# Kernel optimization log

Hardware: AMD Instinct MI355X
Metric: run time of the kernel (lower is better)

The kernel has to match this reference:

```python
import jax, jax.numpy as jnp
import numpy as np

RADIUS = 0.2
NSAMPLE = 32
USE_XYZ = True
NORMALIZE_XYZ = False


def setup_inputs() -> dict:
    key = jax.random.key(0)
    k1, k2, k3 = jax.random.split(key, 3)
    B, N, S, C = 4, 8192, 2048, 64
    xyz = jax.random.uniform(k1, (B, N, 3), dtype=jnp.float32)
    new_xyz = jax.random.uniform(k2, (B, S, 3), dtype=jnp.float32)
    features = jax.random.normal(k3, (B, C, N), dtype=jnp.float32)
    return {"xyz": xyz, "new_xyz": new_xyz, "features": features}


def _ball_query(new_xyz, xyz, radius, nsample):
    # squared distances [B, S, N] via ||q||^2 + ||p||^2 - 2 q.p (no [B,S,N,3] blowup)
    q2 = jnp.sum(new_xyz * new_xyz, axis=-1)  # [B, S]
    p2 = jnp.sum(xyz * xyz, axis=-1)          # [B, N]
    qp = jnp.einsum('bsd,bnd->bsn', new_xyz, xyz)
    d2 = q2[:, :, None] + p2[:, None, :] - 2.0 * qp
    N = xyz.shape[1]
    in_ball = d2 < radius * radius
    # CUDA ball_query semantics: first nsample indices (in original point order)
    # inside the ball; unfilled slots replicate the first found index.
    scores = jnp.where(in_ball, jnp.arange(N, dtype=jnp.int32), jnp.int32(N))
    sorted_idx = -jax.lax.top_k(-scores, nsample)[0]  # ascending smallest scores
    first = sorted_idx[..., :1]
    idx = jnp.where(sorted_idx < N, sorted_idx, first)
    idx = jnp.where(first < N, idx, 0)  # no neighbors at all -> index 0
    return idx  # [B, S, nsample] int32


def _group(features, idx):
    # features [B, C, N], idx [B, S, K] -> [B, C, S, K]
    return jax.vmap(lambda f, i: f[:, i])(features, idx)


def reference(xyz, new_xyz, features):
    idx = _ball_query(new_xyz, xyz, RADIUS, NSAMPLE)
    xyz_t = jnp.transpose(xyz, (0, 2, 1))  # [B, 3, N]
    grouped_xyz = _group(xyz_t, idx)  # [B, 3, S, K]
    grouped_xyz = grouped_xyz - jnp.transpose(new_xyz, (0, 2, 1))[..., None]
    if NORMALIZE_XYZ:
        grouped_xyz = grouped_xyz / RADIUS
    grouped_features = _group(features, idx)  # [B, C, S, K]
    if USE_XYZ:
        return jnp.concatenate([grouped_xyz, grouped_features], axis=1)
    return grouped_features
```

## Files before the change

kernel.cpp:

```cpp
#include <hip/hip_runtime.h>
#include <hip/hip_bf16.h>
#include <stdint.h>

#define BB 4
#define NN 8192
#define SS 2048
#define CC 64
#define NS 32

typedef unsigned short ushort8 __attribute__((ext_vector_type(8)));

__device__ __forceinline__ unsigned short f2bf(float f) {
    union { float ff; unsigned int i; } v; v.ff = f;
    unsigned int x = v.i;
    x += 0x7fffu + ((x >> 16) & 1u);
    return (unsigned short)(x >> 16);
}
__device__ __forceinline__ float bf2f(unsigned short u) {
    union { unsigned int i; float f; } v; v.i = ((unsigned int)u) << 16; return v.f;
}

__global__ void stage(const float* __restrict__ xyz,
                      const float* __restrict__ feat,
                      float4* __restrict__ pts,
                      unsigned short* __restrict__ ft) {
#pragma clang fp contract(off)
    const int t = threadIdx.x;
    if (blockIdx.x < 128) {
        int i = blockIdx.x * 256 + t;
        const float* p = xyz + (size_t)i * 3;
        float x = p[0], y = p[1], z = p[2];
        float p2 = x * x;
        p2 += y * y;
        p2 += z * z;
        pts[i] = make_float4(x, y, z, p2);
        return;
    }
    __shared__ float tile[64][65];
    const int blk = blockIdx.x - 128;
    const int b  = blk >> 7;
    const int n0 = (blk & 127) * 64;
    const float* fb = feat + (size_t)b * CC * NN;
    const int n = t & 63;
    #pragma unroll
    for (int it = 0; it < 16; ++it) {
        int c = it * 4 + (t >> 6);
        tile[n][c] = fb[(size_t)c * NN + n0 + n];
    }
    __syncthreads();
    unsigned short* fo = ft + ((size_t)b * NN + n0) * CC;
    const int c = t & 63;
    #pragma unroll
    for (int it = 0; it < 16; ++it) {
        int r = it * 4 + (t >> 6);
        fo[(size_t)r * CC + c] = f2bf(tile[r][c]);
    }
}

__launch_bounds__(256)
__global__ void bq_group(const float* __restrict__ new_xyz,
                         const float4* __restrict__ pts,
                         const unsigned short* __restrict__ ft,
                         float* __restrict__ out) {
#pragma clang fp contract(off)
    __shared__ unsigned long long wmask[2][4];
    __shared__ int sidx[NS];
    const int t    = threadIdx.x;
    const int wave = t >> 6;
    const int lane = t & 63;
    const int blk  = blockIdx.x;
    const int b    = blk >> 11;
    const int s    = blk & (SS - 1);

    const float* q = new_xyz + (size_t)(b * SS + s) * 3;
    const float qx = q[0], qy = q[1], qz = q[2];
    const float4* pb = pts + (size_t)b * NN;

    float q2 = qx * qx;
    q2 += qy * qy;
    q2 += qz * qz;

    const unsigned long long below = (1ull << lane) - 1ull;
    int have = 0;
    float4 p = pb[t];
    #pragma unroll 1
    for (int base = 0; base < NN; base += 256) {
        float4 pn = pb[(base + 256 < NN) ? (base + 256 + t) : t];
        float qp = qx * p.x;
        qp += qy * p.y;
        qp += qz * p.z;
        float t1 = q2 + p.w;
        float d2 = t1 - 2.0f * qp;
        bool in = d2 < 0.04f;
        unsigned long long m = __ballot(in);
        const int buf = (base >> 8) & 1;
        if (lane == 0) wmask[buf][wave] = m;
        __syncthreads();
        unsigned long long m0 = wmask[buf][0], m1 = wmask[buf][1],
                           m2 = wmask[buf][2], m3 = wmask[buf][3];
        int pre = __popcll(m & below);
        if (wave > 0) pre += __popcll(m0);
        if (wave > 1) pre += __popcll(m1);
        if (wave > 2) pre += __popcll(m2);
        int pos = have + pre;
        if (in && pos < NS) sidx[pos] = base + t;
        have += __popcll(m0) + __popcll(m1) + __popcll(m2) + __popcll(m3);
        if (have >= NS) break;
        p = pn;
    }
    __syncthreads();
    if (have < NS) {
        int first = (have == 0) ? 0 : sidx[0];
        if (t < NS && t >= have)
            sidx[t] = (have == 0) ? 0 : first;
    }
    __syncthreads();

    const int k    = t & 31;
    const int oc   = t >> 5;
    const int idxk = sidx[k];

    const size_t plane = (size_t)SS * NS;
    const size_t ob    = (size_t)b * 67 * plane;
    const size_t so    = (size_t)s * NS + k;

    const unsigned short* fr = ft + ((size_t)b * NN + idxk) * CC + oc * 8;
    ushort8 v = *(const ushort8*)fr;
    float* o = out + ob + (size_t)(3 + oc * 8) * plane + so;
    #pragma unroll
    for (int j = 0; j < 8; ++j)
        o[(size_t)j * plane] = bf2f(v[j]);

    if (t < 96) {
        const int c = t >> 5;
        float4 p3 = pb[idxk];
        float pc = (c == 0) ? p3.x : (c == 1 ? p3.y : p3.z);
        float qc = (c == 0) ? qx : (c == 1 ? qy : qz);
        out[ob + (size_t)c * plane + so] = pc - qc;
    }
}

extern "C" void kernel_launch(void* const* d_in, const int* in_sizes, int n_in,
                              void* d_out, int out_size, void* d_ws, size_t ws_size,
                              hipStream_t stream) {
    const float* xyz     = (const float*)d_in[0];
    const float* new_xyz = (const float*)d_in[1];
    const float* feat    = (const float*)d_in[2];
    for (int i = 0; i < n_in && i < 3; ++i) {
        if (in_sizes[i] == BB * NN * 3)      xyz     = (const float*)d_in[i];
        else if (in_sizes[i] == BB * SS * 3) new_xyz = (const float*)d_in[i];
        else if (in_sizes[i] == BB * CC * NN) feat   = (const float*)d_in[i];
    }
    float* out = (float*)d_out;

    char* ws = (char*)d_ws;
    float4* pts        = (float4*)ws;
    unsigned short* ft = (unsigned short*)(ws + (size_t)BB * NN * sizeof(float4));

    stage<<<640, 256, 0, stream>>>(xyz, feat, pts, ft);
    bq_group<<<BB * SS, 256, 0, stream>>>(new_xyz, pts, ft, out);
}
```

Baseline: 102.0 us.

## Map one query per wavefront and drop block-wide ball-query syncs

Each 256-thread block now handles four queries, one per wavefront, instead of one query per block. Each wave scans 128 points per iteration with two ballots and keeps a per-wave index list, so the shared-mask exchange and __syncthreads in every iteration go away. The gather writes the output with nontemporal stores and 32 channels per lane. The cost is more serial iterations per query and a prefetch that reads past the batch's point array on the last iteration.

```diff
diff --git a/kernel.cpp b/kernel.cpp
--- a/kernel.cpp
+++ b/kernel.cpp
@@ -63,14 +63,13 @@
                          const unsigned short* __restrict__ ft,
                          float* __restrict__ out) {
 #pragma clang fp contract(off)
-    __shared__ unsigned long long wmask[2][4];
-    __shared__ int sidx[NS];
+    __shared__ int sidx[4][NS];
     const int t    = threadIdx.x;
     const int wave = t >> 6;
     const int lane = t & 63;
     const int blk  = blockIdx.x;
-    const int b    = blk >> 11;
-    const int s    = blk & (SS - 1);
+    const int b    = blk >> 9;
+    const int s    = ((blk & 511) << 2) | wave;
 
     const float* q = new_xyz + (size_t)(b * SS + s) * 3;
     const float qx = q[0], qy = q[1], qz = q[2];
@@ -82,61 +81,64 @@
 
     const unsigned long long below = (1ull << lane) - 1ull;
     int have = 0;
-    float4 p = pb[t];
+    float4 p0 = pb[lane];
+    float4 p1 = pb[64 + lane];
     #pragma unroll 1
-    for (int base = 0; base < NN; base += 256) {
-        float4 pn = pb[(base + 256 < NN) ? (base + 256 + t) : t];
-        float qp = qx * p.x;
-        qp += qy * p.y;
-        qp += qz * p.z;
-        float t1 = q2 + p.w;
-        float d2 = t1 - 2.0f * qp;
-        bool in = d2 < 0.04f;
-        unsigned long long m = __ballot(in);
-        const int buf = (base >> 8) & 1;
-        if (lane == 0) wmask[buf][wave] = m;
-        __syncthreads();
-        unsigned long long m0 = wmask[buf][0], m1 = wmask[buf][1],
-                           m2 = wmask[buf][2], m3 = wmask[buf][3];
-        int pre = __popcll(m & below);
-        if (wave > 0) pre += __popcll(m0);
-        if (wave > 1) pre += __popcll(m1);
-        if (wave > 2) pre += __popcll(m2);
-        int pos = have + pre;
-        if (in && pos < NS) sidx[pos] = base + t;
-        have += __popcll(m0) + __popcll(m1) + __popcll(m2) + __popcll(m3);
+    for (int base = 0; base < NN; base += 128) {
+        float4 n0 = pb[base + 128 + lane];
+        float4 n1 = pb[base + 192 + lane];
+        float qp0 = qx * p0.x;
+        qp0 += qy * p0.y;
+        qp0 += qz * p0.z;
+        float t10 = q2 + p0.w;
+        float d20 = t10 - 2.0f * qp0;
+        float qp1 = qx * p1.x;
+        qp1 += qy * p1.y;
+        qp1 += qz * p1.z;
+        float t11 = q2 + p1.w;
+        float d21 = t11 - 2.0f * qp1;
+        bool in0 = d20 < 0.04f;
+        bool in1 = d21 < 0.04f;
+        unsigned long long m0 = __ballot(in0);
+        unsigned long long m1 = __ballot(in1);
+        int c0 = __popcll(m0);
+        int pos0 = have + __popcll(m0 & below);
+        if (in0 && pos0 < NS) sidx[wave][pos0] = base + lane;
+        int pos1 = have + c0 + __popcll(m1 & below);
+        if (in1 && pos1 < NS) sidx[wave][pos1] = base + 64 + lane;
+        have += c0 + __popcll(m1);
         if (have >= NS) break;
-        p = pn;
+        p0 = n0; p1 = n1;
     }
-    __syncthreads();
-    if (have < NS) {
-        int first = (have == 0) ? 0 : sidx[0];
-        if (t < NS && t >= have)
-            sidx[t] = (have == 0) ? 0 : first;
-    }
-    __syncthreads();
+    __builtin_amdgcn_wave_barrier();
 
-    const int k    = t & 31;
-    const int oc   = t >> 5;
-    const int idxk = sidx[k];
+    const int k = lane & 31;
+    const int h = lane >> 5;
+    int idxk;
+    if (k < have) idxk = sidx[wave][k];
+    else          idxk = (have > 0) ? sidx[wave][0] : 0;
 
     const size_t plane = (size_t)SS * NS;
     const size_t ob    = (size_t)b * 67 * plane;
     const size_t so    = (size_t)s * NS + k;
+    float* obase = out + ob + so;
 
-    const unsigned short* fr = ft + ((size_t)b * NN + idxk) * CC + oc * 8;
-    ushort8 v = *(const ushort8*)fr;
-    float* o = out + ob + (size_t)(3 + oc * 8) * plane + so;
+    const unsigned short* fr = ft + ((size_t)b * NN + idxk) * CC + h * 32;
     #pragma unroll
-    for (int j = 0; j < 8; ++j)
-        o[(size_t)j * plane] = bf2f(v[j]);
+    for (int j = 0; j < 4; ++j) {
+        ushort8 v = *(const ushort8*)(fr + j * 8);
+        const int c = 3 + h * 32 + j * 8;
+        #pragma unroll
+        for (int jj = 0; jj < 8; ++jj)
+            __builtin_nontemporal_store(bf2f(v[jj]),
+                                        obase + (size_t)(c + jj) * plane);
+    }
 
-    if (t < 96) {
-        const int c = t >> 5;
+    if (h == 0) {
         float4 p3 = pb[idxk];
-        float pc = (c == 0) ? p3.x : (c == 1 ? p3.y : p3.z);
-        float qc = (c == 0) ? qx : (c == 1 ? qy : qz);
-        out[ob + (size_t)c * plane + so] = pc - qc;
+        __builtin_nontemporal_store(p3.x - qx, obase);
+        __builtin_nontemporal_store(p3.y - qy, obase + plane);
+        __builtin_nontemporal_store(p3.z - qz, obase + 2 * plane);
     }
 }
 
@@ -158,5 +160,5 @@
     unsigned short* ft = (unsigned short*)(ws + (size_t)BB * NN * sizeof(float4));
 
     stage<<<640, 256, 0, stream>>>(xyz, feat, pts, ft);
-    bq_group<<<BB * SS, 256, 0, stream>>>(new_xyz, pts, ft, out);
+    bq_group<<<BB * SS / 4, 256, 0, stream>>>(new_xyz, pts, ft, out);
 }
```

Measured after the change: 101.8 us. No clear change (-0.2%).
